# Kernel tuning notes

Hardware: AMD Instinct MI355X
Metric: run time of the kernel (lower is better)

The kernel has to match this reference:

```python
import jax, jax.numpy as jnp
import numpy as np

N = 65536       # n_nodes
E = 1048576     # n_edges (avg degree 16)
IDX = 256       # index_size
DIN = 512       # gcn_input_size
DH = 512        # gcn_hidden_size
DOUT = 128      # gcn_output_size
S = 256         # sample_size


def gcn_conv(h, W, b, src, dst, n):
    # PyG GCNConv: linear, add self-loops, symmetric deg^-1/2 normalization, scatter-add.
    h = h @ W
    loop = jnp.arange(n)
    s = jnp.concatenate([src, loop])
    d = jnp.concatenate([dst, loop])
    deg = jax.ops.segment_sum(jnp.ones(s.shape[0], h.dtype), d, num_segments=n)
    inv_sqrt = jax.lax.rsqrt(deg)  # deg >= 1 due to self-loops
    norm = inv_sqrt[s] * inv_sqrt[d]
    out = jax.ops.segment_sum(h[s] * norm[:, None], d, num_segments=n)
    return out + b


def _lin_init(k, fan_in, shape):
    bound = 1.0 / np.sqrt(fan_in)
    return jax.random.uniform(k, shape, jnp.float32, -bound, bound)


def setup_inputs() -> dict:
    key = jax.random.key(0)
    ks = jax.random.split(key, 14)
    x = jax.random.normal(ks[0], (N, IDX + 768), jnp.float32)
    edge_index = jax.random.randint(ks[1], (2, E), 0, N, dtype=jnp.int64)
    return {
        "x": x,
        "W_t1": _lin_init(ks[2], IDX, (IDX, DIN)),
        "b_t1": _lin_init(ks[3], IDX, (DIN,)),
        "W_t2": _lin_init(ks[4], 768, (768, DIN)),
        "b_t2": _lin_init(ks[5], 768, (DIN,)),
        "W1": _lin_init(ks[6], DIN, (DIN, DH)),
        "b1": _lin_init(ks[7], DIN, (DH,)),
        "W2": _lin_init(ks[8], DH, (DH, DOUT)),
        "b2": _lin_init(ks[9], DH, (DOUT,)),
        "matrix": jax.random.normal(ks[10], (DOUT, DOUT), jnp.float32),
        "lin_w": _lin_init(ks[11], 1, (2,)),   # nn.Linear(1, 2) weight, squeezed
        "lin_b": _lin_init(ks[12], 1, (2,)),
        "edge_index": edge_index,
    }


def reference(x, W_t1, b_t1, W_t2, b_t2, W1, b1, W2, b2, matrix, lin_w, lin_b, edge_index):
    src, dst = edge_index[0], edge_index[1]
    # dual-input linear fusion
    h = x[:, :IDX] @ W_t1 + b_t1 + x[:, IDX:] @ W_t2 + b_t2
    h = gcn_conv(h, W1, b1, src, dst, N)
    h = jax.nn.relu(h)  # dropout is identity in eval mode
    h = gcn_conv(h, W2, b2, src, dst, N)
    # per-sample bilinear score, batched over chunks
    e = h.reshape(N // S, S, DOUT)
    scores = jnp.einsum('bid,de,bje->bij', e, matrix, e)  # [B, S, S]
    out = scores[..., None] * lin_w + lin_b               # Linear(1, 2)
    return out.reshape(-1, 2)
```

## Files before the change

kernel.cpp:

```cpp
#include <hip/hip_runtime.h>
#include <stdint.h>

#define NN 65536

typedef __attribute__((ext_vector_type(8))) short bf16x8;
typedef __attribute__((ext_vector_type(4))) float f32x4;

__device__ __forceinline__ unsigned short f2bf(float f) {
    unsigned u = __float_as_uint(f);
    u += 0x7fffu + ((u >> 16) & 1u);
    return (unsigned short)(u >> 16);
}
__device__ __forceinline__ float bf2f(unsigned short h) { return __uint_as_float(((unsigned)h) << 16); }
__device__ __forceinline__ float blo(unsigned u) { return __uint_as_float(u << 16); }
__device__ __forceinline__ float bhi(unsigned u) { return __uint_as_float(u & 0xffff0000u); }
__device__ __forceinline__ unsigned pack2(float a, float b) {
    return ((unsigned)f2bf(b) << 16) | (unsigned)f2bf(a);
}
__device__ __forceinline__ unsigned trunc2(float x, float y) {
    return __builtin_amdgcn_perm(__float_as_uint(y), __float_as_uint(x), 0x07060302u);
}

__device__ __forceinline__ void gl_lds16(const void* g, void* l) {
    __builtin_amdgcn_global_load_lds((const __attribute__((address_space(1))) void*)g,
                                     (__attribute__((address_space(3))) void*)l, 16, 0, 0);
}

__global__ void prep_pack(const float* Wt1, const float* Wt2, const float* W1,
                          const float* W2, const float* Mtx,
                          unsigned short* Wcat, unsigned short* W1T,
                          unsigned short* W2T, unsigned short* MTh, unsigned short* MTl) {
    int i = blockIdx.x * 256 + threadIdx.x;
    if (i < 524288) {
        int k = i >> 9, j = i & 511;
        float v = (k < 256) ? Wt1[k * 512 + j] : Wt2[(k - 256) * 512 + j];
        Wcat[i] = f2bf(v);
    } else if (i < 786432) {
        int t = i - 524288; int n = t >> 9, j = t & 511;
        W1T[t] = f2bf(W1[j * 512 + n]);
    } else if (i < 851968) {
        int t = i - 786432; int n = t >> 9, j = t & 511;
        W2T[t] = f2bf(W2[j * 128 + n]);
    } else if (i < 868352) {
        int t = i - 851968; int d = t >> 7, e = t & 127;
        float m = Mtx[e * 128 + d];
        unsigned short h = f2bf(m);
        MTh[t] = h; MTl[t] = f2bf(m - bf2f(h));
    }
}

__global__ void cbias_k(const float* bt1, const float* bt2, const float* W1, float* c) {
    __shared__ float sm[256];
    int t = threadIdx.x;
    int n = blockIdx.x * 32 + (t & 31);
    int jp = t >> 5;
    float acc = 0.f;
    for (int j = jp * 64; j < jp * 64 + 64; j++)
        acc += (bt1[j] + bt2[j]) * W1[j * 512 + n];
    sm[t] = acc;
    __syncthreads();
    if (t < 32) {
        float a = 0.f;
#pragma unroll
        for (int p = 0; p < 8; p++) a += sm[p * 32 + t];
        c[blockIdx.x * 32 + t] = a;
    }
}

__global__ void count_k(const int* dst, int* cnt, int E) {
    int e = blockIdx.x * 256 + threadIdx.x;
    if (e < E) atomicAdd(&cnt[dst[e]], 1);
}
__global__ void red_k(const int* cnt, int* bsum) {
    __shared__ int sm[256];
    int tid = threadIdx.x;
    sm[tid] = cnt[blockIdx.x * 256 + tid];
    __syncthreads();
    for (int s = 128; s > 0; s >>= 1) {
        if (tid < s) sm[tid] += sm[tid + s];
        __syncthreads();
    }
    if (tid == 0) bsum[blockIdx.x] = sm[0];
}
__global__ void scanb_k(const int* bsum, int* boff) {
    __shared__ int sm[256];
    int tid = threadIdx.x;
    int v0 = bsum[tid];
    sm[tid] = v0;
    __syncthreads();
    for (int s = 1; s < 256; s <<= 1) {
        int t = sm[tid];
        if (tid >= s) t += sm[tid - s];
        __syncthreads();
        sm[tid] = t;
        __syncthreads();
    }
    boff[tid] = sm[tid] - v0;
}
__global__ void scanf_k(const int* cnt, const int* boff, int* rowptr, int* cursor, float* invs) {
    __shared__ int sm[256];
    int tid = threadIdx.x;
    int i = blockIdx.x * 256 + tid;
    int v = cnt[i];
    sm[tid] = v;
    __syncthreads();
    for (int s = 1; s < 256; s <<= 1) {
        int t = sm[tid];
        if (tid >= s) t += sm[tid - s];
        __syncthreads();
        sm[tid] = t;
        __syncthreads();
    }
    int incl = sm[tid];
    int base = boff[blockIdx.x];
    int excl = base + incl - v;
    rowptr[i] = excl;
    cursor[i] = excl;
    invs[i] = rsqrtf((float)(v + 1));
    if (i == NN - 1) rowptr[NN] = base + incl;
}
__global__ void fill_k(const int* src, const int* dst, int* cursor, int* colv, int E) {
    int e = blockIdx.x * 256 + threadIdx.x;
    if (e < E) {
        int d = dst[e];
        int p = atomicAdd(&cursor[d], 1);
        colv[p] = src[e];
    }
}

__global__ __launch_bounds__(256, 2) void gemm_bt(const unsigned short* A, const unsigned short* BT,
                                                  unsigned short* C, const float* bias,
                                                  const float* rs,
                                                  int M, int N, int K) {
    __shared__ __align__(16) unsigned short sA[128 * 32];
    __shared__ __align__(16) unsigned short sB[128 * 32];
    int tid = threadIdx.x, wave = tid >> 6, lane = tid & 63;
    int bm = blockIdx.y * 128, bn = blockIdx.x * 128;
    int wm = (wave >> 1) * 64, wn = (wave & 1) * 64;
    f32x4 acc[4][4];
#pragma unroll
    for (int i = 0; i < 4; i++)
#pragma unroll
        for (int j = 0; j < 4; j++) acc[i][j] = (f32x4){0.f, 0.f, 0.f, 0.f};
    int sr = wave * 32 + (lane >> 2);
    int sc = (lane & 3) * 8;
    const int fr = lane & 15;
    const int fk = (lane >> 4) * 8;
    for (int k0 = 0; k0 < K; k0 += 32) {
        const unsigned short* ga = A + (size_t)(bm + sr) * K + k0 + sc;
        gl_lds16(ga, &sA[sr * 32 + sc]);
        gl_lds16(ga + (size_t)16 * K, &sA[(sr + 16) * 32 + sc]);
        const unsigned short* gb = BT + (size_t)(bn + sr) * K + k0 + sc;
        gl_lds16(gb, &sB[sr * 32 + sc]);
        gl_lds16(gb + (size_t)16 * K, &sB[(sr + 16) * 32 + sc]);
        __syncthreads();
        bf16x8 af[4], bfr[4];
#pragma unroll
        for (int i = 0; i < 4; i++) af[i] = *(const bf16x8*)&sA[(wm + i * 16 + fr) * 32 + fk];
#pragma unroll
        for (int j = 0; j < 4; j++) bfr[j] = *(const bf16x8*)&sB[(wn + j * 16 + fr) * 32 + fk];
#pragma unroll
        for (int i = 0; i < 4; i++)
#pragma unroll
            for (int j = 0; j < 4; j++)
                acc[i][j] = __builtin_amdgcn_mfma_f32_16x16x32_bf16(af[i], bfr[j], acc[i][j], 0, 0, 0);
        __syncthreads();
    }
    int rq = (lane >> 4) * 4;
#pragma unroll
    for (int i = 0; i < 4; i++)
#pragma unroll
        for (int j = 0; j < 4; j++) {
            int col = bn + wn + j * 16 + fr;
            float bb = bias ? bias[col] : 0.f;
#pragma unroll
            for (int r = 0; r < 4; r++) {
                int row = bm + wm + i * 16 + rq + r;
                float scale = rs ? rs[row] : 1.f;
                C[(size_t)row * N + col] = f2bf((acc[i][j][r] + bb) * scale);
            }
        }
}

__global__ __launch_bounds__(256, 2) void gemm_f32a(const float* A, const unsigned short* BT,
                                                    unsigned short* C, const float* bias,
                                                    const float* rs) {
    const int K = 1024, N = 512;
    __shared__ __align__(16) float sAf[128 * 32];
    __shared__ __align__(16) unsigned short sB[128 * 32];
    int tid = threadIdx.x, wave = tid >> 6, lane = tid & 63;
    int b = blockIdx.x;
    int xcd = b & 7, jn = (b >> 3) & 3, tt = b >> 5;
    int bm = (tt * 8 + xcd) * 128, bn = jn * 128;
    int wm = (wave >> 1) * 64, wn = (wave & 1) * 64;
    f32x4 acc[4][4];
#pragma unroll
    for (int i = 0; i < 4; i++)
#pragma unroll
        for (int j = 0; j < 4; j++) acc[i][j] = (f32x4){0.f, 0.f, 0.f, 0.f};
    int sr = wave * 32 + (lane >> 2);
    int sc = (lane & 3) * 8;
    int arow = lane >> 3;
    int achk = (lane & 7) ^ arow;
    const int fr = lane & 15;
    const int fk = (lane >> 4) * 8;
    const float* Abase = A + (size_t)(bm + wave * 32 + arow) * K + achk * 4;
    const unsigned short* Bbase = BT + (size_t)(bn + sr) * K + sc;
    for (int k0 = 0; k0 < K; k0 += 32) {
#pragma unroll
        for (int i = 0; i < 4; i++)
            gl_lds16(Abase + (size_t)(8 * i) * K + k0, &sAf[(wave * 32 + i * 8) * 32]);
        gl_lds16(Bbase + k0, &sB[sr * 32 + sc]);
        gl_lds16(Bbase + (size_t)16 * K + k0, &sB[(sr + 16) * 32 + sc]);
        __syncthreads();
        bf16x8 af[4], bfr[4];
#pragma unroll
        for (int i = 0; i < 4; i++) {
            int r = wm + i * 16 + fr;
            int s = r & 7;
            int c0 = fk >> 2;
            float4 fa = *(const float4*)&sAf[r * 32 + ((c0 ^ s) << 2)];
            float4 fb = *(const float4*)&sAf[r * 32 + (((c0 + 1) ^ s) << 2)];
            union { unsigned u[4]; bf16x8 v; } t;
            t.u[0] = trunc2(fa.x, fa.y);
            t.u[1] = trunc2(fa.z, fa.w);
            t.u[2] = trunc2(fb.x, fb.y);
            t.u[3] = trunc2(fb.z, fb.w);
            af[i] = t.v;
        }
#pragma unroll
        for (int j = 0; j < 4; j++) bfr[j] = *(const bf16x8*)&sB[(wn + j * 16 + fr) * 32 + fk];
#pragma unroll
        for (int i = 0; i < 4; i++)
#pragma unroll
            for (int j = 0; j < 4; j++)
                acc[i][j] = __builtin_amdgcn_mfma_f32_16x16x32_bf16(af[i], bfr[j], acc[i][j], 0, 0, 0);
        __syncthreads();
    }
    int rq = (lane >> 4) * 4;
#pragma unroll
    for (int i = 0; i < 4; i++)
#pragma unroll
        for (int j = 0; j < 4; j++) {
            int col = bn + wn + j * 16 + fr;
            float bb = bias[col];
#pragma unroll
            for (int r = 0; r < 4; r++) {
                int row = bm + wm + i * 16 + rq + r;
                C[(size_t)row * N + col] = f2bf((acc[i][j][r] + bb) * rs[row]);
            }
        }
}

__global__ __launch_bounds__(256, 2) void gemm_T(const unsigned short* h2h, const unsigned short* h2l,
                                                 const unsigned short* MTh, const unsigned short* MTl,
                                                 unsigned short* Th, unsigned short* Tl) {
    __shared__ __align__(16) unsigned short sA[128 * 32];
    __shared__ __align__(16) unsigned short sB[128 * 32];
    int tid = threadIdx.x, wave = tid >> 6, lane = tid & 63;
    int bm = blockIdx.x * 128;
    int wm = (wave >> 1) * 64, wn = (wave & 1) * 64;
    f32x4 acc[4][4];
#pragma unroll
    for (int i = 0; i < 4; i++)
#pragma unroll
        for (int j = 0; j < 4; j++) acc[i][j] = (f32x4){0.f, 0.f, 0.f, 0.f};
    int sr = wave * 32 + (lane >> 2);
    int sc = (lane & 3) * 8;
    const int fr = lane & 15;
    const int fk = (lane >> 4) * 8;
    const unsigned short* APs[3] = {h2h, h2h, h2l};
    const unsigned short* BPs[3] = {MTh, MTl, MTh};
    for (int it = 0; it < 12; it++) {
        int ph = it >> 2, k0 = (it & 3) * 32;
        const unsigned short* ga = APs[ph] + (size_t)(bm + sr) * 128 + k0 + sc;
        gl_lds16(ga, &sA[sr * 32 + sc]);
        gl_lds16(ga + 16 * 128, &sA[(sr + 16) * 32 + sc]);
        const unsigned short* gb = BPs[ph] + (size_t)sr * 128 + k0 + sc;
        gl_lds16(gb, &sB[sr * 32 + sc]);
        gl_lds16(gb + 16 * 128, &sB[(sr + 16) * 32 + sc]);
        __syncthreads();
        bf16x8 af[4], bfr[4];
#pragma unroll
        for (int i = 0; i < 4; i++) af[i] = *(const bf16x8*)&sA[(wm + i * 16 + fr) * 32 + fk];
#pragma unroll
        for (int j = 0; j < 4; j++) bfr[j] = *(const bf16x8*)&sB[(wn + j * 16 + fr) * 32 + fk];
#pragma unroll
        for (int i = 0; i < 4; i++)
#pragma unroll
            for (int j = 0; j < 4; j++)
                acc[i][j] = __builtin_amdgcn_mfma_f32_16x16x32_bf16(af[i], bfr[j], acc[i][j], 0, 0, 0);
        __syncthreads();
    }
    int rq = (lane >> 4) * 4;
#pragma unroll
    for (int i = 0; i < 4; i++)
#pragma unroll
        for (int j = 0; j < 4; j++) {
            int col = wn + j * 16 + fr;
#pragma unroll
            for (int r = 0; r < 4; r++) {
                int row = bm + wm + i * 16 + rq + r;
                float v = acc[i][j][r];
                unsigned short h = f2bf(v);
                Th[(size_t)row * 128 + col] = h;
                Tl[(size_t)row * 128 + col] = f2bf(v - bf2f(h));
            }
        }
}

__global__ __launch_bounds__(256) void agg512(const unsigned short* t, const int* rowptr,
                                              const int* colv, const float* invs,
                                              const float* bias, unsigned short* outp) {
    int wave = threadIdx.x >> 6, lane = threadIdx.x & 63;
    int node = blockIdx.x * 4 + wave;
    int d0 = lane * 8;
    float acc[8] = {0.f, 0.f, 0.f, 0.f, 0.f, 0.f, 0.f, 0.f};
    int r0 = rowptr[node], r1 = rowptr[node + 1];
    uint4 sv = *(const uint4*)&t[(size_t)node * 512 + d0];
    float wd = invs[node];
    int e = r0;
    for (; e + 8 <= r1; e += 8) {
        int s[8];
#pragma unroll
        for (int c = 0; c < 8; c++) s[c] = colv[e + c];
        uint4 v[8];
#pragma unroll
        for (int c = 0; c < 8; c++) v[c] = *(const uint4*)&t[(size_t)s[c] * 512 + d0];
#pragma unroll
        for (int c = 0; c < 8; c++) {
            acc[0] += blo(v[c].x); acc[1] += bhi(v[c].x);
            acc[2] += blo(v[c].y); acc[3] += bhi(v[c].y);
            acc[4] += blo(v[c].z); acc[5] += bhi(v[c].z);
            acc[6] += blo(v[c].w); acc[7] += bhi(v[c].w);
        }
    }
    if (e + 4 <= r1) {
        int s[4];
#pragma unroll
        for (int c = 0; c < 4; c++) s[c] = colv[e + c];
        uint4 v[4];
#pragma unroll
        for (int c = 0; c < 4; c++) v[c] = *(const uint4*)&t[(size_t)s[c] * 512 + d0];
#pragma unroll
        for (int c = 0; c < 4; c++) {
            acc[0] += blo(v[c].x); acc[1] += bhi(v[c].x);
            acc[2] += blo(v[c].y); acc[3] += bhi(v[c].y);
            acc[4] += blo(v[c].z); acc[5] += bhi(v[c].z);
            acc[6] += blo(v[c].w); acc[7] += bhi(v[c].w);
        }
        e += 4;
    }
    for (; e < r1; e++) {
        uint4 v = *(const uint4*)&t[(size_t)colv[e] * 512 + d0];
        acc[0] += blo(v.x); acc[1] += bhi(v.x);
        acc[2] += blo(v.y); acc[3] += bhi(v.y);
        acc[4] += blo(v.z); acc[5] += bhi(v.z);
        acc[6] += blo(v.w); acc[7] += bhi(v.w);
    }
    acc[0] += blo(sv.x); acc[1] += bhi(sv.x);
    acc[2] += blo(sv.y); acc[3] += bhi(sv.y);
    acc[4] += blo(sv.z); acc[5] += bhi(sv.z);
    acc[6] += blo(sv.w); acc[7] += bhi(sv.w);
    float o[8];
#pragma unroll
    for (int k = 0; k < 8; k++) {
        float v = acc[k] * wd + bias[d0 + k];
        o[k] = v > 0.f ? v : 0.f;
    }
    uint4 pv;
    pv.x = pack2(o[0], o[1]); pv.y = pack2(o[2], o[3]);
    pv.z = pack2(o[4], o[5]); pv.w = pack2(o[6], o[7]);
    *(uint4*)&outp[(size_t)node * 512 + d0] = pv;
}

__global__ __launch_bounds__(256) void agg128(const unsigned short* u, const int* rowptr,
                                              const int* colv, const float* invs,
                                              const float* bias, unsigned short* h2h, unsigned short* h2l) {
    int wave = threadIdx.x >> 6, lane = threadIdx.x & 63;
    int node = blockIdx.x * 4 + wave;
    int q = lane >> 4, ql = lane & 15;
    int d0 = ql * 8;
    float acc[8] = {0.f, 0.f, 0.f, 0.f, 0.f, 0.f, 0.f, 0.f};
    int r0 = rowptr[node], r1 = rowptr[node + 1];
    uint4 sv = *(const uint4*)&u[(size_t)node * 128 + d0];
    float wd = invs[node];
    int e = r0 + q;
    for (; e + 4 < r1; e += 8) {
        int s0 = colv[e], s1 = colv[e + 4];
        uint4 v0 = *(const uint4*)&u[(size_t)s0 * 128 + d0];
        uint4 v1 = *(const uint4*)&u[(size_t)s1 * 128 + d0];
        acc[0] += blo(v0.x) + blo(v1.x); acc[1] += bhi(v0.x) + bhi(v1.x);
        acc[2] += blo(v0.y) + blo(v1.y); acc[3] += bhi(v0.y) + bhi(v1.y);
        acc[4] += blo(v0.z) + blo(v1.z); acc[5] += bhi(v0.z) + bhi(v1.z);
        acc[6] += blo(v0.w) + blo(v1.w); acc[7] += bhi(v0.w) + bhi(v1.w);
    }
    if (e < r1) {
        uint4 v = *(const uint4*)&u[(size_t)colv[e] * 128 + d0];
        acc[0] += blo(v.x); acc[1] += bhi(v.x);
        acc[2] += blo(v.y); acc[3] += bhi(v.y);
        acc[4] += blo(v.z); acc[5] += bhi(v.z);
        acc[6] += blo(v.w); acc[7] += bhi(v.w);
    }
#pragma unroll
    for (int k = 0; k < 8; k++) {
        acc[k] += __shfl_xor(acc[k], 16);
        acc[k] += __shfl_xor(acc[k], 32);
    }
    float sf[8] = {blo(sv.x), bhi(sv.x), blo(sv.y), bhi(sv.y), blo(sv.z), bhi(sv.z), blo(sv.w), bhi(sv.w)};
    unsigned short hh[8], hl[8];
#pragma unroll
    for (int k = 0; k < 8; k++) {
        float v = (acc[k] + sf[k]) * wd + bias[d0 + k];
        hh[k] = f2bf(v);
        hl[k] = f2bf(v - bf2f(hh[k]));
    }
    if (q == 0) {
        uint4 ph, pl;
        ph.x = ((unsigned)hh[1] << 16) | hh[0]; ph.y = ((unsigned)hh[3] << 16) | hh[2];
        ph.z = ((unsigned)hh[5] << 16) | hh[4]; ph.w = ((unsigned)hh[7] << 16) | hh[6];
        pl.x = ((unsigned)hl[1] << 16) | hl[0]; pl.y = ((unsigned)hl[3] << 16) | hl[2];
        pl.z = ((unsigned)hl[5] << 16) | hl[4]; pl.w = ((unsigned)hl[7] << 16) | hl[6];
        *(uint4*)&h2h[(size_t)node * 128 + d0] = ph;
        *(uint4*)&h2l[(size_t)node * 128 + d0] = pl;
    }
}

__global__ __launch_bounds__(256, 2) void bilinear_k(const unsigned short* Th, const unsigned short* Tl,
                                                     const unsigned short* Eh, const float* lin_w,
                                                     const float* lin_b, float* outp) {
    int tid = threadIdx.x, wave = tid >> 6, lane = tid & 63;
    int b = blockIdx.x >> 1, half = blockIdx.x & 1;
    int fr = lane & 15, q = lane >> 4;
    int irow0 = b * 256 + half * 128 + wave * 32;
    bf16x8 Ah[2][4], Al[2][4];
#pragma unroll
    for (int it = 0; it < 2; it++)
#pragma unroll
        for (int kk = 0; kk < 4; kk++) {
            size_t off = (size_t)(irow0 + it * 16 + fr) * 128 + kk * 32 + q * 8;
            Ah[it][kk] = *(const bf16x8*)&Th[off];
            Al[it][kk] = *(const bf16x8*)&Tl[off];
        }
    float w0 = lin_w[0], w1 = lin_w[1], c0 = lin_b[0], c1 = lin_b[1];
    for (int jt = 0; jt < 16; jt++) {
        bf16x8 Bf[4];
#pragma unroll
        for (int kk = 0; kk < 4; kk++)
            Bf[kk] = *(const bf16x8*)&Eh[(size_t)(b * 256 + jt * 16 + fr) * 128 + kk * 32 + q * 8];
#pragma unroll
        for (int it = 0; it < 2; it++) {
            f32x4 acc = (f32x4){0.f, 0.f, 0.f, 0.f};
#pragma unroll
            for (int kk = 0; kk < 4; kk++) {
                acc = __builtin_amdgcn_mfma_f32_16x16x32_bf16(Ah[it][kk], Bf[kk], acc, 0, 0, 0);
                acc = __builtin_amdgcn_mfma_f32_16x16x32_bf16(Al[it][kk], Bf[kk], acc, 0, 0, 0);
            }
#pragma unroll
            for (int r = 0; r < 4; r++) {
                int iloc = half * 128 + wave * 32 + it * 16 + q * 4 + r;
                int jloc = jt * 16 + fr;
                size_t o = ((size_t)b * 65536 + (size_t)iloc * 256 + jloc) * 2;
                float s = acc[r];
                float2 ov;
                ov.x = fmaf(s, w0, c0);
                ov.y = fmaf(s, w1, c1);
                *(float2*)&outp[o] = ov;
            }
        }
    }
}

extern "C" void kernel_launch(void* const* d_in, const int* in_sizes, int n_in,
                              void* d_out, int out_size, void* d_ws, size_t ws_size,
                              hipStream_t stream) {
    const float* x   = (const float*)d_in[0];
    const float* Wt1 = (const float*)d_in[1];
    const float* bt1 = (const float*)d_in[2];
    const float* Wt2 = (const float*)d_in[3];
    const float* bt2 = (const float*)d_in[4];
    const float* W1  = (const float*)d_in[5];
    const float* b1  = (const float*)d_in[6];
    const float* W2  = (const float*)d_in[7];
    const float* b2  = (const float*)d_in[8];
    const float* Mtx = (const float*)d_in[9];
    const float* lw  = (const float*)d_in[10];
    const float* lb  = (const float*)d_in[11];
    const int*   ei  = (const int*)d_in[12];
    int E = in_sizes[12] / 2;
    const int* srcp = ei;
    const int* dstp = ei + E;

    unsigned char* p = (unsigned char*)d_ws;
    size_t off = 0;
    auto alloc = [&](size_t bytes) -> void* {
        void* r = p + off;
        off = (off + bytes + 255) & ~(size_t)255;
        return r;
    };
    int*   cnt    = (int*)alloc((size_t)NN * 4);
    int*   rowptr = (int*)alloc(((size_t)NN + 1) * 4);
    int*   cursor = (int*)alloc((size_t)NN * 4);
    float* invs   = (float*)alloc((size_t)NN * 4);
    int*   bsum   = (int*)alloc(256 * 4);
    int*   boff   = (int*)alloc(256 * 4);
    int*   colv   = (int*)alloc((size_t)E * 4);
    unsigned short* Wcat   = (unsigned short*)alloc(524288 * 2);
    unsigned short* W1T    = (unsigned short*)alloc(262144 * 2);
    unsigned short* W2T    = (unsigned short*)alloc(65536 * 2);
    unsigned short* MTh    = (unsigned short*)alloc(16384 * 2);
    unsigned short* MTl    = (unsigned short*)alloc(16384 * 2);
    float*          cbias  = (float*)alloc(512 * 4);
    unsigned short* WcombT = (unsigned short*)alloc(524288 * 2);
    unsigned short* t1     = (unsigned short*)alloc((size_t)NN * 512 * 2);
    unsigned short* h1     = (unsigned short*)alloc((size_t)NN * 512 * 2);
    unsigned short* uu     = (unsigned short*)alloc((size_t)NN * 128 * 2);
    unsigned short* Th  = t1;
    unsigned short* Tl  = t1 + (size_t)NN * 128;
    unsigned short* h2h = h1;
    unsigned short* h2l = h1 + (size_t)NN * 128;

    hipMemsetAsync(cnt, 0, (size_t)NN * 4, stream);
    prep_pack<<<3392, 256, 0, stream>>>(Wt1, Wt2, W1, W2, Mtx, Wcat, W1T, W2T, MTh, MTl);
    cbias_k<<<16, 256, 0, stream>>>(bt1, bt2, W1, cbias);
    count_k<<<(E + 255) / 256, 256, 0, stream>>>(dstp, cnt, E);
    red_k<<<256, 256, 0, stream>>>(cnt, bsum);
    scanb_k<<<1, 256, 0, stream>>>(bsum, boff);
    scanf_k<<<256, 256, 0, stream>>>(cnt, boff, rowptr, cursor, invs);
    fill_k<<<(E + 255) / 256, 256, 0, stream>>>(srcp, dstp, cursor, colv, E);
    gemm_bt<<<dim3(8, 4), 256, 0, stream>>>(W1T, Wcat, WcombT, nullptr, nullptr, 512, 1024, 512);
    gemm_f32a<<<2048, 256, 0, stream>>>(x, WcombT, t1, cbias, invs);
    agg512<<<NN / 4, 256, 0, stream>>>(t1, rowptr, colv, invs, b1, h1);
    gemm_bt<<<dim3(1, 512), 256, 0, stream>>>(h1, W2T, uu, nullptr, invs, NN, 128, 512);
    agg128<<<NN / 4, 256, 0, stream>>>(uu, rowptr, colv, invs, b2, h2h, h2l);
    gemm_T<<<512, 256, 0, stream>>>(h2h, h2l, MTh, MTl, Th, Tl);
    bilinear_k<<<512, 256, 0, stream>>>(Th, Tl, h2h, lw, lb, (float*)d_out);
}
```

Before: 912.8 us.

## Double-buffer f32-input GEMM with register prefetch and bf16 LDS staging

Reworks the fp32-A GEMM main loop into a two-stage pipeline. The next A tile is prefetched into registers, truncated to bf16 and written to a padded LDS buffer, while the B tile for the next step is loaded asynchronously into a second buffer. Both overlap with the MFMA work on the current buffer, which removes one barrier per iteration and halves the A shared-memory footprint per stage. In exchange it uses more registers for the prefetched float4s and relies on padding rather than the XOR swizzle to avoid bank conflicts.

```diff
diff --git a/kernel.cpp b/kernel.cpp
--- a/kernel.cpp
+++ b/kernel.cpp
@@ -186,8 +186,8 @@
                                                     unsigned short* C, const float* bias,
                                                     const float* rs) {
     const int K = 1024, N = 512;
-    __shared__ __align__(16) float sAf[128 * 32];
-    __shared__ __align__(16) unsigned short sB[128 * 32];
+    __shared__ __align__(16) unsigned short sA[2][128 * 40];
+    __shared__ __align__(16) unsigned short sB[2][128 * 32];
     int tid = threadIdx.x, wave = tid >> 6, lane = tid & 63;
     int b = blockIdx.x;
     int xcd = b & 7, jn = (b >> 3) & 3, tt = b >> 5;
@@ -200,43 +200,70 @@
         for (int j = 0; j < 4; j++) acc[i][j] = (f32x4){0.f, 0.f, 0.f, 0.f};
     int sr = wave * 32 + (lane >> 2);
     int sc = (lane & 3) * 8;
-    int arow = lane >> 3;
-    int achk = (lane & 7) ^ arow;
+    const unsigned short* Bbase = BT + (size_t)(bn + sr) * K + sc;
+    int arow = tid >> 1, ahalf = tid & 1;
+    const float* Abase = A + (size_t)(bm + arow) * K + ahalf * 16;
+    unsigned short* wptr = &sA[0][0] + arow * 40 + ahalf * 16;
     const int fr = lane & 15;
     const int fk = (lane >> 4) * 8;
-    const float* Abase = A + (size_t)(bm + wave * 32 + arow) * K + achk * 4;
-    const unsigned short* Bbase = BT + (size_t)(bn + sr) * K + sc;
+
+    float4 la0, la1, la2, la3;
+#define LDA(k0)                                        \
+    do {                                               \
+        const float* ap = Abase + (k0);                \
+        la0 = *(const float4*)(ap);                    \
+        la1 = *(const float4*)(ap + 4);                \
+        la2 = *(const float4*)(ap + 8);                \
+        la3 = *(const float4*)(ap + 12);               \
+    } while (0)
+#define GLB(k0, c)                                                         \
+    do {                                                                   \
+        gl_lds16(Bbase + (k0), &sB[c][sr * 32 + sc]);                      \
+        gl_lds16(Bbase + (size_t)16 * K + (k0), &sB[c][(sr + 16) * 32 + sc]); \
+    } while (0)
+#define PACKW(c)                                                 \
+    do {                                                         \
+        union { unsigned u[8]; uint4 q[2]; } t;                  \
+        t.u[0] = trunc2(la0.x, la0.y);                           \
+        t.u[1] = trunc2(la0.z, la0.w);                           \
+        t.u[2] = trunc2(la1.x, la1.y);                           \
+        t.u[3] = trunc2(la1.z, la1.w);                           \
+        t.u[4] = trunc2(la2.x, la2.y);                           \
+        t.u[5] = trunc2(la2.z, la2.w);                           \
+        t.u[6] = trunc2(la3.x, la3.y);                           \
+        t.u[7] = trunc2(la3.z, la3.w);                           \
+        unsigned short* dst = wptr + (c) * (128 * 40);           \
+        *(uint4*)dst = t.q[0];                                   \
+        *(uint4*)(dst + 8) = t.q[1];                             \
+    } while (0)
+
+    LDA(0);
+    GLB(0, 0);
+    PACKW(0);
+    __syncthreads();
     for (int k0 = 0; k0 < K; k0 += 32) {
-#pragma unroll
-        for (int i = 0; i < 4; i++)
-            gl_lds16(Abase + (size_t)(8 * i) * K + k0, &sAf[(wave * 32 + i * 8) * 32]);
-        gl_lds16(Bbase + k0, &sB[sr * 32 + sc]);
-        gl_lds16(Bbase + (size_t)16 * K + k0, &sB[(sr + 16) * 32 + sc]);
-        __syncthreads();
+        int c = (k0 >> 5) & 1;
+        bool more = (k0 + 32 < K);
+        if (more) {
+            LDA(k0 + 32);
+            GLB(k0 + 32, c ^ 1);
+        }
         bf16x8 af[4], bfr[4];
 #pragma unroll
-        for (int i = 0; i < 4; i++) {
-            int r = wm + i * 16 + fr;
-            int s = r & 7;
-            int c0 = fk >> 2;
-            float4 fa = *(const float4*)&sAf[r * 32 + ((c0 ^ s) << 2)];
-            float4 fb = *(const float4*)&sAf[r * 32 + (((c0 + 1) ^ s) << 2)];
-            union { unsigned u[4]; bf16x8 v; } t;
-            t.u[0] = trunc2(fa.x, fa.y);
-            t.u[1] = trunc2(fa.z, fa.w);
-            t.u[2] = trunc2(fb.x, fb.y);
-            t.u[3] = trunc2(fb.z, fb.w);
-            af[i] = t.v;
-        }
-#pragma unroll
-        for (int j = 0; j < 4; j++) bfr[j] = *(const bf16x8*)&sB[(wn + j * 16 + fr) * 32 + fk];
+        for (int i = 0; i < 4; i++) af[i] = *(const bf16x8*)&sA[c][(wm + i * 16 + fr) * 40 + fk];
+#pragma unroll
+        for (int j = 0; j < 4; j++) bfr[j] = *(const bf16x8*)&sB[c][(wn + j * 16 + fr) * 32 + fk];
 #pragma unroll
         for (int i = 0; i < 4; i++)
 #pragma unroll
             for (int j = 0; j < 4; j++)
                 acc[i][j] = __builtin_amdgcn_mfma_f32_16x16x32_bf16(af[i], bfr[j], acc[i][j], 0, 0, 0);
-        __syncthreads();
-    }
+        if (more) PACKW(c ^ 1);
+        __syncthreads();
+    }
+#undef LDA
+#undef GLB
+#undef PACKW
     int rq = (lane >> 4) * 4;
 #pragma unroll
     for (int i = 0; i < 4; i++)
```

Result: no change. 930.3 us (+1.9%).
